# Kernel tuning notes

Measured on AMD Instinct MI355X. Metric: run time of the kernel, lower is better.

Reference implementation:

```python
import jax, jax.numpy as jnp
import numpy as np

MIN_NORM = 1e-15
C = 1.0            # Poincare ball curvature (geoopt default c=1.0)
SQRT_C = C ** 0.5
EPS_PROJ = 4e-3    # geoopt float32 ball projection epsilon
KERNEL = 3


def _project(x):
    # geoopt PoincareBall projx: clip points to radius (1-eps)/sqrt(c)
    norm = jnp.maximum(jnp.linalg.norm(x, axis=-1, keepdims=True), MIN_NORM)
    maxnorm = (1.0 - EPS_PROJ) / SQRT_C
    return jnp.where(norm > maxnorm, x / norm * maxnorm, x)


def _expmap0(u):
    u_norm = jnp.maximum(jnp.linalg.norm(u, axis=-1, keepdims=True), MIN_NORM)
    gamma = jnp.tanh(jnp.clip(SQRT_C * u_norm, -15.0, 15.0)) * u / (SQRT_C * u_norm)
    return _project(gamma)


def setup_inputs() -> dict:
    key = jax.random.key(0)
    k1, k2, k3 = jax.random.split(key, 3)
    M, B, D, O = 27000, 16, 64, 128  # M = 30^3 voxel positions
    x = jax.random.normal(k1, (M, B, D), dtype=jnp.float32) * 0.3
    # keep points strictly inside the Poincare ball
    n = jnp.linalg.norm(x, axis=-1, keepdims=True)
    x = x * (0.8 * jnp.tanh(n) / jnp.maximum(n, 1e-6))
    # kaiming_normal_(a=sqrt(5)) on (O, D): std = sqrt(2/(1+5))/sqrt(fan_in)
    std = (2.0 / 6.0) ** 0.5 / D ** 0.5
    weight_v = jax.random.normal(k2, (O, D), dtype=jnp.float32) * std
    bound = 4.0 / D ** 0.5
    bias_b = jax.random.uniform(k3, (O, 1), dtype=jnp.float32, minval=-bound, maxval=bound)
    return {"x": x, "weight_v": weight_v, "bias_b": bias_b}


def _gyroplane_conv(x, weight_v, bias_b):
    # x: [sampled_dim=M, batch=B, manifold_dim=D]
    M, B, D = x.shape
    O = weight_v.shape[0]
    N = int(round(M ** (1.0 / 3.0)))
    s = KERNEL // 2
    grid = jnp.transpose(x, (1, 0, 2)).reshape(B, N, N, N, D)
    grid = jnp.pad(grid, ((0, 0), (s, s), (s, s), (s, s), (0, 0)))  # zero pad (origin of ball)
    Np = N + 2 * s
    xp = grid.reshape(B, Np ** 3, D)

    # gyroplane parameters (RiemannianLayer properties)
    p = _expmap0(weight_v * bias_b)                       # bias point on ball, (O, D)
    p2 = jnp.sum(p * p, axis=-1)                          # (O,)
    a = weight_v * jnp.maximum(1.0 - C * p2, MIN_NORM)[:, None]  # transp0(p, _weight), (O, D)

    # normdist2plane(x, p, a, signed=True): diff = mobius_add(-p, x)
    # mobius_add(-p, x) = [alpha*(-p) + beta*x] / den  with
    #   alpha = 1 - 2c<p,x> + c|x|^2, beta = 1 - c|p|^2,
    #   den   = 1 - 2c<p,x> + c^2 |p|^2 |x|^2
    # expand dot products to avoid materializing (B, Mp, O, D)
    x2 = jnp.sum(xp * xp, axis=-1)                        # (B, Mp)
    xdotp = jnp.einsum('bmd,od->bmo', xp, p)              # (B, Mp, O)
    xdota = jnp.einsum('bmd,od->bmo', xp, a)              # (B, Mp, O)
    pa = jnp.sum(p * a, axis=-1)                          # (O,)

    alpha = 1.0 - 2.0 * C * xdotp + C * x2[..., None]
    beta = 1.0 - C * p2                                   # (O,)
    den = jnp.maximum(1.0 - 2.0 * C * xdotp + (C * C) * p2 * x2[..., None], MIN_NORM)

    sc_diff_a = (-alpha * pa + beta * xdota) / den        # <diff, a>, signed
    diff_norm2 = jnp.maximum(
        (alpha * alpha * p2 - 2.0 * alpha * beta * xdotp + beta * beta * x2[..., None]) / (den * den),
        MIN_NORM)
    a_norm = jnp.maximum(jnp.sqrt(jnp.sum(a * a, axis=-1)), MIN_NORM)  # (O,)

    num = 2.0 * SQRT_C * sc_diff_a
    denom = jnp.maximum((1.0 - C * diff_norm2) * a_norm, MIN_NORM)
    dist = jnp.arcsinh(num / denom) / SQRT_C              # (B, Mp, O)

    # sum of per-point distances over each 3x3x3 patch == box filter
    dist = dist.reshape(B, Np, Np, Np, O)
    out = jnp.zeros((B, N, N, N, O), dist.dtype)
    for di in range(KERNEL):
        for dj in range(KERNEL):
            for dk in range(KERNEL):
                out = out + dist[:, di:di + N, dj:dj + N, dk:dk + N, :]
    return jnp.transpose(out, (0, 4, 1, 2, 3))            # (B, O, N, N, N)


def reference(x, weight_v, bias_b):
    return _gyroplane_conv(x, weight_v, bias_b)
```

## Files before the change

### kernel.cpp

```cpp
#include <hip/hip_runtime.h>
#include <math.h>

#define NB 16
#define NO 128
#define ND 64
#define NN 30
#define NM 27000
#define PROW 32
#define PPLANE 960
#define PML 28800

typedef _Float16 half8 __attribute__((ext_vector_type(8)));
typedef _Float16 half4 __attribute__((ext_vector_type(4)));
typedef float    f32x4 __attribute__((ext_vector_type(4)));

__device__ __forceinline__ float asinh_fast(float t) {
    return __logf(t + __builtin_amdgcn_sqrtf(t * t + 1.0f));
}

__device__ __forceinline__ float gyro_dist(float x2, float dp, float da,
                                           float p2, float pa, float an) {
    float beta  = 1.0f - p2;
    float alpha = 1.0f - 2.0f * dp + x2;
    float den   = fmaxf(1.0f - 2.0f * dp + p2 * x2, 1e-15f);
    float rden  = __builtin_amdgcn_rcpf(den);
    float sc    = (beta * da - alpha * pa) * rden;
    float dn2   = fmaxf((alpha * alpha * p2 - 2.0f * alpha * beta * dp +
                         beta * beta * x2) * (rden * rden), 1e-15f);
    float denom = fmaxf((1.0f - dn2) * an, 1e-15f);
    float t     = 2.0f * sc * __builtin_amdgcn_rcpf(denom);
    return asinh_fast(t);
}

__device__ __forceinline__ void param_scalars(float S, float bb,
                                              float* fp_o, float* p2_o,
                                              float* betaC_o, float* pa_o,
                                              float* an_o) {
    float sq  = sqrtf(S);
    float un  = fmaxf(fabsf(bb) * sq, 1e-15f);
    float t1  = tanhf(fminf(un, 15.0f));
    float sc1 = t1 / un;
    float gn  = fmaxf(t1, 1e-15f);
    float sc2 = (gn > 0.996f) ? (0.996f / gn) : 1.0f;
    float fp  = bb * sc1 * sc2;
    float p2  = fp * fp * S;
    float betaC = fmaxf(1.0f - p2, 1e-15f);
    *fp_o = fp; *p2_o = p2; *betaC_o = betaC;
    *pa_o = fp * betaC * S;
    *an_o = fmaxf(betaC * sq, 1e-15f);
}

__device__ __forceinline__ void dist0_wave(const float* __restrict__ w,
                                           const float* __restrict__ bias,
                                           int o, int tid, float* out_lds) {
    if (tid < 64) {
        float v = w[o * ND + tid];
        float s = v * v;
#pragma unroll
        for (int off = 32; off > 0; off >>= 1) s += __shfl_xor(s, off, 64);
        if (tid == 0) {
            float fp, p2, betaC, pa, an;
            param_scalars(s, bias[o], &fp, &p2, &betaC, &pa, &an);
            float dn2   = fmaxf(p2, 1e-15f);
            float denom = fmaxf((1.0f - dn2) * an, 1e-15f);
            *out_lds = asinh_fast(-2.0f * pa * __builtin_amdgcn_rcpf(denom));
        }
    }
}

__global__ __launch_bounds__(128) void gyro_params_k(
    const float* __restrict__ w, const float* __restrict__ bias,
    _Float16* __restrict__ pfg, _Float16* __restrict__ afg,
    float* __restrict__ p2g, float* __restrict__ pag,
    float* __restrict__ ang) {
    int o = threadIdx.x;
    const float* wr = w + o * ND;
    float bb = bias[o];
    float S = 0.0f;
    for (int d = 0; d < ND; ++d) S += wr[d] * wr[d];
    float fp, p2, betaC, pa, an;
    param_scalars(S, bb, &fp, &p2, &betaC, &pa, &an);
    p2g[o] = p2; pag[o] = pa; ang[o] = an;

    half8* pf8 = (half8*)pfg;
    half8* af8 = (half8*)afg;
    int ot8 = o >> 4, j = o & 15;
#pragma unroll
    for (int h = 0; h < 2; ++h)
#pragma unroll
        for (int q = 0; q < 4; ++q) {
            int d0i = h * 32 + q * 8;
            half8 hp, ha;
#pragma unroll
            for (int jj = 0; jj < 8; ++jj) {
                float wv = wr[d0i + jj];
                hp[jj] = (_Float16)(wv * fp);
                ha[jj] = (_Float16)(wv * betaC);
            }
            pf8[(ot8 * 2 + h) * 64 + j + 16 * q] = hp;
            af8[(ot8 * 2 + h) * 64 + j + 16 * q] = ha;
        }
}

__global__ __launch_bounds__(256) void gyro_dist_mfma_h(
    const float* __restrict__ x,
    const _Float16* __restrict__ pfg, const _Float16* __restrict__ afg,
    const float* __restrict__ p2g, const float* __restrict__ pag,
    const float* __restrict__ ang,
    _Float16* __restrict__ tmp) {
    __shared__ __align__(16) half8 xf[8 * 64];
    __shared__ float x2p[64 * 8];
    __shared__ __align__(16) float x2_s[64];

    const int tid = threadIdx.x;
    const int mp0 = blockIdx.x * 64;
    const int b   = blockIdx.y;
    const int lane = tid & 63, wid = tid >> 6;

    const half8* pf8 = (const half8*)pfg;
    const half8* af8 = (const half8*)afg;
    half8 bp[2][2], ba[2][2];
#pragma unroll
    for (int ot = 0; ot < 2; ++ot)
#pragma unroll
        for (int h = 0; h < 2; ++h) {
            int idx = ((wid * 2 + ot) * 2 + h) * 64 + lane;
            bp[ot][h] = pf8[idx];
            ba[ot][h] = af8[idx];
        }

#pragma unroll
    for (int n = 0; n < 2; ++n) {
        int s = tid + n * 256;
        int f = s >> 6, l = s & 63;
        int mt = f >> 1, h = f & 1;
        int mloc = mt * 16 + (l & 15);
        int quad = l >> 4;
        int k0 = h * 32 + quad * 8;
        int gmp = mp0 + mloc;
        int kcol = gmp & 31;
        int row  = gmp >> 5;
        half8 hv;
        float part = 0.0f;
        if (kcol < 30) {
            int gm = row * 30 + kcol;
            const float4* src = (const float4*)(x + ((size_t)gm * NB + b) * ND + k0);
            float4 v0 = src[0], v1 = src[1];
            float vv[8] = {v0.x, v0.y, v0.z, v0.w, v1.x, v1.y, v1.z, v1.w};
#pragma unroll
            for (int jj = 0; jj < 8; ++jj) {
                hv[jj] = (_Float16)vv[jj];
                part += vv[jj] * vv[jj];
            }
        } else {
#pragma unroll
            for (int jj = 0; jj < 8; ++jj) hv[jj] = (_Float16)0.0f;
        }
        xf[f * 64 + l] = hv;
        x2p[mloc * 8 + h * 4 + quad] = part;
    }
    __syncthreads();
    if (tid < 64) {
        float s = 0.0f;
#pragma unroll
        for (int r = 0; r < 8; ++r) s += x2p[tid * 8 + r];
        x2_s[tid] = s;
    }
    __syncthreads();

    f32x4 accp[4][2], acca[4][2];
#pragma unroll
    for (int mt = 0; mt < 4; ++mt)
#pragma unroll
        for (int ot = 0; ot < 2; ++ot) {
            accp[mt][ot] = (f32x4)0.0f;
            acca[mt][ot] = (f32x4)0.0f;
        }
#pragma unroll
    for (int h = 0; h < 2; ++h) {
        half8 afr[4];
#pragma unroll
        for (int mt = 0; mt < 4; ++mt) afr[mt] = xf[(mt * 2 + h) * 64 + lane];
#pragma unroll
        for (int mt = 0; mt < 4; ++mt)
#pragma unroll
            for (int ot = 0; ot < 2; ++ot) {
                accp[mt][ot] = __builtin_amdgcn_mfma_f32_16x16x32_f16(
                    afr[mt], bp[ot][h], accp[mt][ot], 0, 0, 0);
                acca[mt][ot] = __builtin_amdgcn_mfma_f32_16x16x32_f16(
                    afr[mt], ba[ot][h], acca[mt][ot], 0, 0, 0);
            }
    }

    const int lo = lane & 15, quad = lane >> 4;
    const size_t obase = (size_t)(b * NO) * PML;
#pragma unroll
    for (int ot = 0; ot < 2; ++ot) {
        const int o = wid * 32 + ot * 16 + lo;
        const float P2 = p2g[o], PA = pag[o], AN = ang[o];
        const float denom0 = fmaxf((1.0f - fmaxf(P2, 1e-15f)) * AN, 1e-15f);
        const float d0 = asinh_fast(-2.0f * PA * __builtin_amdgcn_rcpf(denom0));
        float dv[4][4];
#pragma unroll
        for (int mt = 0; mt < 4; ++mt) {
            const int mb = mt * 16 + quad * 4;
            float4 x2v = *(const float4*)&x2_s[mb];
            dv[mt][0] = gyro_dist(x2v.x, accp[mt][ot][0], acca[mt][ot][0], P2, PA, AN);
            dv[mt][1] = gyro_dist(x2v.y, accp[mt][ot][1], acca[mt][ot][1], P2, PA, AN);
            dv[mt][2] = gyro_dist(x2v.z, accp[mt][ot][2], acca[mt][ot][2], P2, PA, AN);
            dv[mt][3] = gyro_dist(x2v.w, accp[mt][ot][3], acca[mt][ot][3], P2, PA, AN);
        }
#pragma unroll
        for (int mt = 0; mt < 4; ++mt) {
            float tl = __shfl_up(dv[mt][3], 16);
            float tr = __shfl_down(dv[mt][0], 16);
            float L, R;
            if (mt & 1) {
                float tl2 = __shfl_down(dv[mt - 1][3], 48);
                L = (quad == 0) ? tl2 : tl;
                R = (quad == 3) ? d0 : tr;
            } else {
                float tr2 = __shfl_up(dv[mt + 1][0], 48);
                L = (quad == 0) ? d0 : tl;
                R = (quad == 3) ? tr2 : tr;
            }
            half4 hv;
            hv[0] = (_Float16)(L + dv[mt][0] + dv[mt][1]);
            hv[1] = (_Float16)(dv[mt][0] + dv[mt][1] + dv[mt][2]);
            hv[2] = (_Float16)(dv[mt][1] + dv[mt][2] + dv[mt][3]);
            hv[3] = (_Float16)(dv[mt][2] + dv[mt][3] + R);
            *(half4*)(tmp + obase + (size_t)o * PML + (mp0 + mt * 16 + quad * 4)) = hv;
        }
    }
}

__global__ __launch_bounds__(256) void gyro_box3d_h(
    const _Float16* __restrict__ tmp, float* __restrict__ dst,
    const float* __restrict__ w, const float* __restrict__ bias) {
    __shared__ __align__(16) float vin[10 * PPLANE];
    __shared__ float d0sh;

    const int tid = threadIdx.x;
    const int i0  = blockIdx.x * 8;
    const int o   = blockIdx.y;
    const int b   = blockIdx.z;
    const int bo  = b * NO + o;

    dist0_wave(w, bias, o, tid, &d0sh);
    __syncthreads();
    const float d0 = d0sh;
    const float T3 = 3.0f * d0;
    float4* vin4 = (float4*)vin;

    const half8* tsrc = (const half8*)(tmp + (size_t)bo * PML);
    for (int idx = tid; idx < 1200; idx += 256) {
        int sl = idx / 120, r8 = idx - sl * 120;
        int ip = i0 - 1 + sl;
        float f[8];
        if (ip >= 0 && ip < NN) {
            half8 hv = tsrc[ip * 120 + r8];
#pragma unroll
            for (int jj = 0; jj < 8; ++jj) f[jj] = (float)hv[jj];
        } else {
#pragma unroll
            for (int jj = 0; jj < 8; ++jj) f[jj] = T3;
        }
        int o4 = (sl * PPLANE + r8 * 8) >> 2;
        float4 v0; v0.x = f[0]; v0.y = f[1]; v0.z = f[2]; v0.w = f[3];
        float4 v1; v1.x = f[4]; v1.y = f[5]; v1.z = f[6]; v1.w = f[7];
        vin4[o4] = v0; vin4[o4 + 1] = v1;
    }
    __syncthreads();

    float4 st[10];

#pragma unroll
    for (int n = 0; n < 10; ++n) {
        int q = tid + n * 256;
        if (q < 2400) {
            int rem = q % 240;
            int j = rem >> 3;
            float4 cc = vin4[q];
            float4 up, dn;
            if (j == 0)  { up.x = T3; up.y = T3; up.z = T3; up.w = T3; }
            else         up = vin4[q - 8];
            if (j == 29) { dn.x = T3; dn.y = T3; dn.z = T3; dn.w = T3; }
            else         dn = vin4[q + 8];
            float4 s;
            s.x = cc.x + up.x + dn.x; s.y = cc.y + up.y + dn.y;
            s.z = cc.z + up.z + dn.z; s.w = cc.w + up.w + dn.w;
            st[n] = s;
        }
    }
    __syncthreads();
#pragma unroll
    for (int n = 0; n < 10; ++n) {
        int q = tid + n * 256;
        if (q < 2400) vin4[q] = st[n];
    }
    __syncthreads();

    const int nout = (NN - i0 < 8) ? (NN - i0) : 8;
    for (int q = tid; q < nout * 240; q += 256) {
        int pl = q / 240, rem = q - pl * 240;
        int j = rem >> 3, c = rem & 7;
        int o4 = (pl + 1) * 240 + rem;
        float4 a = vin4[o4 - 240], m = vin4[o4], e = vin4[o4 + 240];
        float4 s;
        s.x = a.x + m.x + e.x; s.y = a.y + m.y + e.y;
        s.z = a.z + m.z + e.z; s.w = a.w + m.w + e.w;
        int i = i0 + pl;
        float* g = dst + (size_t)bo * NM + i * 900 + j * 30 + c * 4;
        float2 lo2; lo2.x = s.x; lo2.y = s.y;
        *(float2*)g = lo2;
        if (c < 7) {
            float2 hi2; hi2.x = s.z; hi2.y = s.w;
            *(float2*)(g + 2) = hi2;
        }
    }
}

extern "C" void kernel_launch(void* const* d_in, const int* in_sizes, int n_in,
                              void* d_out, int out_size, void* d_ws, size_t ws_size,
                              hipStream_t stream) {
    const float* x    = (const float*)d_in[0];
    const float* w    = (const float*)d_in[1];
    const float* bias = (const float*)d_in[2];
    float* out = (float*)d_out;

    _Float16* pfg = (_Float16*)d_ws;
    _Float16* afg = (_Float16*)((char*)d_ws + 16384);
    float* p2g = (float*)((char*)d_ws + 32768);
    float* pag = (float*)((char*)d_ws + 33280);
    float* ang = (float*)((char*)d_ws + 33792);
    _Float16* tmp = (_Float16*)((char*)d_ws + 36864);

    gyro_params_k<<<1, 128, 0, stream>>>(w, bias, pfg, afg, p2g, pag, ang);

    dim3 gD(PML / 64, NB);
    gyro_dist_mfma_h<<<gD, 256, 0, stream>>>(x, pfg, afg, p2g, pag, ang, tmp);

    dim3 gB(4, NO, NB);
    gyro_box3d_h<<<gB, 256, 0, stream>>>(tmp, out, w, bias);
}
```

Measured before the change: 438.3 us.

## Restructure box filter with fp16 LDS and register-rolling i-axis sums

The 3D box-filter kernel now keeps its staged slab in LDS as fp16 instead of fp32, which halves shared memory. Each of 240 threads walks the i-axis with a rolling window of three j-summed rows held in registers, replacing the two-pass LDS rewrite and two of the barriers. The per-block border constant is now computed redundantly by every wave through shuffles, which removes an LDS broadcast and a sync. In exchange, only 240 of 256 threads do the output work and the loop over planes runs serially per thread.

```diff
diff --git a/kernel.cpp b/kernel.cpp
--- a/kernel.cpp
+++ b/kernel.cpp
@@ -50,22 +50,17 @@
     *an_o = fmaxf(betaC * sq, 1e-15f);
 }
 
-__device__ __forceinline__ void dist0_wave(const float* __restrict__ w,
+__device__ __forceinline__ float dist0_all(const float* __restrict__ w,
                                            const float* __restrict__ bias,
-                                           int o, int tid, float* out_lds) {
-    if (tid < 64) {
-        float v = w[o * ND + tid];
-        float s = v * v;
-#pragma unroll
-        for (int off = 32; off > 0; off >>= 1) s += __shfl_xor(s, off, 64);
-        if (tid == 0) {
-            float fp, p2, betaC, pa, an;
-            param_scalars(s, bias[o], &fp, &p2, &betaC, &pa, &an);
-            float dn2   = fmaxf(p2, 1e-15f);
-            float denom = fmaxf((1.0f - dn2) * an, 1e-15f);
-            *out_lds = asinh_fast(-2.0f * pa * __builtin_amdgcn_rcpf(denom));
-        }
-    }
+                                           int o, int lane) {
+    float v = w[o * ND + lane];
+    float s = v * v;
+#pragma unroll
+    for (int off = 32; off > 0; off >>= 1) s += __shfl_xor(s, off, 64);
+    float fp, p2, betaC, pa, an;
+    param_scalars(s, bias[o], &fp, &p2, &betaC, &pa, &an);
+    float denom = fmaxf((1.0f - fmaxf(p2, 1e-15f)) * an, 1e-15f);
+    return asinh_fast(-2.0f * pa * __builtin_amdgcn_rcpf(denom));
 }
 
 __global__ __launch_bounds__(128) void gyro_params_k(
@@ -234,88 +229,83 @@
     }
 }
 
-__global__ __launch_bounds__(256) void gyro_box3d_h(
+__global__ __launch_bounds__(256) void gyro_box_i_h(
     const _Float16* __restrict__ tmp, float* __restrict__ dst,
     const float* __restrict__ w, const float* __restrict__ bias) {
-    __shared__ __align__(16) float vin[10 * PPLANE];
-    __shared__ float d0sh;
-
-    const int tid = threadIdx.x;
-    const int i0  = blockIdx.x * 8;
-    const int o   = blockIdx.y;
-    const int b   = blockIdx.z;
-    const int bo  = b * NO + o;
-
-    dist0_wave(w, bias, o, tid, &d0sh);
-    __syncthreads();
-    const float d0 = d0sh;
+    __shared__ __align__(16) _Float16 vol[10 * PPLANE];
+
+    const int tid  = threadIdx.x;
+    const int lane = tid & 63;
+    const int i0   = blockIdx.x * 8;
+    const int o    = blockIdx.y;
+    const int b    = blockIdx.z;
+    const int bo   = b * NO + o;
+
+    const float d0 = dist0_all(w, bias, o, lane);
     const float T3 = 3.0f * d0;
-    float4* vin4 = (float4*)vin;
+    const _Float16 T3h = (_Float16)T3;
 
     const half8* tsrc = (const half8*)(tmp + (size_t)bo * PML);
+    half8* v8 = (half8*)vol;
     for (int idx = tid; idx < 1200; idx += 256) {
         int sl = idx / 120, r8 = idx - sl * 120;
         int ip = i0 - 1 + sl;
-        float f[8];
+        half8 hv;
         if (ip >= 0 && ip < NN) {
-            half8 hv = tsrc[ip * 120 + r8];
-#pragma unroll
-            for (int jj = 0; jj < 8; ++jj) f[jj] = (float)hv[jj];
+            hv = tsrc[ip * 120 + r8];
         } else {
 #pragma unroll
-            for (int jj = 0; jj < 8; ++jj) f[jj] = T3;
-        }
-        int o4 = (sl * PPLANE + r8 * 8) >> 2;
-        float4 v0; v0.x = f[0]; v0.y = f[1]; v0.z = f[2]; v0.w = f[3];
-        float4 v1; v1.x = f[4]; v1.y = f[5]; v1.z = f[6]; v1.w = f[7];
-        vin4[o4] = v0; vin4[o4 + 1] = v1;
+            for (int jj = 0; jj < 8; ++jj) hv[jj] = T3h;
+        }
+        v8[idx] = hv;
     }
     __syncthreads();
 
-    float4 st[10];
-
-#pragma unroll
-    for (int n = 0; n < 10; ++n) {
-        int q = tid + n * 256;
-        if (q < 2400) {
-            int rem = q % 240;
-            int j = rem >> 3;
-            float4 cc = vin4[q];
-            float4 up, dn;
-            if (j == 0)  { up.x = T3; up.y = T3; up.z = T3; up.w = T3; }
-            else         up = vin4[q - 8];
-            if (j == 29) { dn.x = T3; dn.y = T3; dn.z = T3; dn.w = T3; }
-            else         dn = vin4[q + 8];
+    if (tid < 240) {
+        const int j = tid >> 3, g = tid & 7;
+        const half4* vb = (const half4*)vol;
+        const int base = j * 8 + g;
+
+        auto jsum = [&](int sl) -> float4 {
+            const half4* pb = vb + sl * 240;
+            half4 c = pb[base];
             float4 s;
-            s.x = cc.x + up.x + dn.x; s.y = cc.y + up.y + dn.y;
-            s.z = cc.z + up.z + dn.z; s.w = cc.w + up.w + dn.w;
-            st[n] = s;
-        }
-    }
-    __syncthreads();
-#pragma unroll
-    for (int n = 0; n < 10; ++n) {
-        int q = tid + n * 256;
-        if (q < 2400) vin4[q] = st[n];
-    }
-    __syncthreads();
-
-    const int nout = (NN - i0 < 8) ? (NN - i0) : 8;
-    for (int q = tid; q < nout * 240; q += 256) {
-        int pl = q / 240, rem = q - pl * 240;
-        int j = rem >> 3, c = rem & 7;
-        int o4 = (pl + 1) * 240 + rem;
-        float4 a = vin4[o4 - 240], m = vin4[o4], e = vin4[o4 + 240];
-        float4 s;
-        s.x = a.x + m.x + e.x; s.y = a.y + m.y + e.y;
-        s.z = a.z + m.z + e.z; s.w = a.w + m.w + e.w;
-        int i = i0 + pl;
-        float* g = dst + (size_t)bo * NM + i * 900 + j * 30 + c * 4;
-        float2 lo2; lo2.x = s.x; lo2.y = s.y;
-        *(float2*)g = lo2;
-        if (c < 7) {
-            float2 hi2; hi2.x = s.z; hi2.y = s.w;
-            *(float2*)(g + 2) = hi2;
+            s.x = (float)c[0]; s.y = (float)c[1];
+            s.z = (float)c[2]; s.w = (float)c[3];
+            if (j > 0) {
+                half4 u = pb[base - 8];
+                s.x += (float)u[0]; s.y += (float)u[1];
+                s.z += (float)u[2]; s.w += (float)u[3];
+            } else {
+                s.x += T3; s.y += T3; s.z += T3; s.w += T3;
+            }
+            if (j < NN - 1) {
+                half4 dn = pb[base + 8];
+                s.x += (float)dn[0]; s.y += (float)dn[1];
+                s.z += (float)dn[2]; s.w += (float)dn[3];
+            } else {
+                s.x += T3; s.y += T3; s.z += T3; s.w += T3;
+            }
+            return s;
+        };
+
+        const int nout = (NN - i0 < 8) ? (NN - i0) : 8;
+        float4 a = jsum(0);
+        float4 bc = jsum(1);
+        float* gbase = dst + (size_t)bo * NM + j * 30 + g * 4;
+        for (int p = 0; p < nout; ++p) {
+            float4 c = jsum(p + 2);
+            float4 s;
+            s.x = a.x + bc.x + c.x; s.y = a.y + bc.y + c.y;
+            s.z = a.z + bc.z + c.z; s.w = a.w + bc.w + c.w;
+            float* gp = gbase + (size_t)(i0 + p) * 900;
+            float2 lo2; lo2.x = s.x; lo2.y = s.y;
+            *(float2*)gp = lo2;
+            if (g < 7) {
+                float2 hi2; hi2.x = s.z; hi2.y = s.w;
+                *(float2*)(gp + 2) = hi2;
+            }
+            a = bc; bc = c;
         }
     }
 }
@@ -341,5 +331,5 @@
     gyro_dist_mfma_h<<<gD, 256, 0, stream>>>(x, pfg, afg, p2g, pag, ang, tmp);
 
     dim3 gB(4, NO, NB);
-    gyro_box3d_h<<<gB, 256, 0, stream>>>(tmp, out, w, bias);
-}
+    gyro_box_i_h<<<gB, 256, 0, stream>>>(tmp, out, w, bias);
+}
```

Measured after the change: 423.0 us. -3.5%, faster.
